# Kernel tuning notes

Hardware: AMD Instinct MI355X
Metric: run time of the kernel (lower is better)

## Reference

```python
import jax, jax.numpy as jnp
import numpy as np

L = 32        # label_num = len(label2idx)
SOS = 0       # label2idx['[SOS]']
END = 1       # label2idx['[END]']
NEG = -10000.0
B, T = 512, 1024


def setup_inputs() -> dict:
    key = jax.random.key(0)
    k1, k2, k3 = jax.random.split(key, 3)
    emission = jax.random.normal(k1, (B, T, L), dtype=jnp.float32)
    label_ids = jax.random.randint(k2, (B, T), 0, L)
    transitions = jax.random.normal(k3, (L, L), dtype=jnp.float32)
    # CrfLayer.__init__: forbid transitions into [SOS] and out of [END]
    transitions = transitions.at[SOS, :].set(NEG).at[:, END].set(NEG)
    return {"emission": emission, "label_ids": label_ids, "transitions": transitions}


def reference(emission, label_ids, transitions):
    b, t, l = emission.shape
    # ---- _forward_alg: log-partition via sequential logsumexp recurrence ----
    alpha0 = jnp.full((b, l), NEG, dtype=emission.dtype).at[:, SOS].set(0.0)
    feats_t = jnp.transpose(emission, (1, 0, 2))  # [T, B, L]

    def step(alpha, feat):
        # aa[b, j, i] = alpha[b, i] + feat[b, j] + transitions[j, i]
        aa = alpha[:, None, :] + feat[:, :, None] + transitions[None, :, :]
        return jax.nn.logsumexp(aa, axis=2), None

    alpha, _ = jax.lax.scan(step, alpha0, feats_t)
    forward_score = jax.nn.logsumexp(alpha + transitions[END][None, :], axis=1)  # [B]

    # ---- _score_sentence: score of the gold path ----
    tags = jnp.concatenate(
        [jnp.full((b, 1), SOS, dtype=label_ids.dtype), label_ids], axis=1)  # [B, T+1]
    trans_score = transitions[tags[:, 1:], tags[:, :-1]].sum(axis=1)          # [B]
    emit_score = jnp.take_along_axis(
        emission, tags[:, 1:, None].astype(jnp.int32), axis=2)[..., 0].sum(axis=1)  # [B]
    gold_score = trans_score + emit_score + transitions[END, tags[:, -1]]

    # loss = sum(forward_score - gold_score)
    return jnp.sum(forward_score - gold_score)
```

## Files before the change

### kernel.cpp

```cpp
#include <hip/hip_runtime.h>


typedef float  f32x16 __attribute__((ext_vector_type(16)));
typedef short  s16x8  __attribute__((ext_vector_type(8)));
typedef float  f32x2  __attribute__((ext_vector_type(2)));
typedef float  f32x4  __attribute__((ext_vector_type(4)));

#define TT 1024
#define LL 32
#define BB 512
#define NW 4
#define CH 8
#define CL 128
#define MS 33

union Frag { s16x8 v; unsigned u[4]; };

__device__ __forceinline__ unsigned pack_bf16(float lo, float hi) {
    return __builtin_amdgcn_perm(__float_as_uint(hi), __float_as_uint(lo), 0x07060302u);
}

__global__ __launch_bounds__(NW * 64, 2) void crf_fused_kernel(
    const float* __restrict__ emission,
    const int*   __restrict__ label_ids,
    const float* __restrict__ transitions,
    float*       __restrict__ out)
{
    __shared__ __align__(16) float shM[CH][32 * MS];
    __shared__ __align__(16) float shF[CH][32];
    __shared__ float shQ[2][64];
    __shared__ float tgArr[NW];
    __shared__ int   capArr[CH];

    const int tid  = threadIdx.x;
    const int w    = tid >> 6;
    const int lane = tid & 63;
    const int j    = lane & 31;
    const int h    = lane >> 5;
    const int b    = blockIdx.x;
    const int t0   = w * (2 * CL);

    {
        const int* labB = label_ids + b * TT + t0;
        float g = 0.0f;
#pragma unroll
        for (int u = 0; u < 4; ++u) {
            int tt = t0 + 64 * u + lane;
            int l1 = labB[64 * u + lane];
            int l0 = (tt == 0) ? 0 : label_ids[b * TT + tt - 1];
            g += transitions[(l1 << 5) + l0];
            g += emission[((size_t)b * TT + tt) * LL + l1];
            if (tt == TT - 1) g += transitions[32 + l1];
        }
#pragma unroll
        for (int m = 32; m >= 1; m >>= 1) g += __shfl_xor(g, m, 64);
        if (lane == 0) tgArr[w] = g;
    }

    const float* trow = transitions + j * 32;
    Frag Ea0, Ea1;
#pragma unroll
    for (int p = 0; p < 4; ++p) {
        int c0 = ((2 * p) & 3)     + 8 * ((2 * p) >> 2)     + 4 * h;
        int c1 = ((2 * p + 1) & 3) + 8 * ((2 * p + 1) >> 2) + 4 * h;
        Ea0.u[p] = pack_bf16(__expf(trow[c0]),      __expf(trow[c1]));
        Ea1.u[p] = pack_bf16(__expf(trow[16 + c0]), __expf(trow[16 + c1]));
    }

    Frag B0a, B1a, B0b, B1b;
#pragma unroll
    for (int i = 0; i < 8; ++i) {
        int row = (i & 3) + 8 * (i >> 2) + 4 * h;
        short lo = (short)((row == j)      ? 0x3F80 : 0);
        short hi = (short)((row + 16 == j) ? 0x3F80 : 0);
        B0a.v[i] = lo;  B1a.v[i] = hi;
        B0b.v[i] = lo;  B1b.v[i] = hi;
    }

    f32x16 zc, accA, accB;
#pragma unroll
    for (int i = 0; i < 16; ++i) zc[i] = 0.0f;

    const float* emA  = emission + ((size_t)b * TT + t0) * LL + j;
    const float* emBp = emA + (size_t)CL * LL;

    float ringA[8], ringB[8];
#pragma unroll
    for (int s = 0; s < 8; ++s) { ringA[s] = emA[s * LL]; ringB[s] = emBp[s * LL]; }

    shF[2 * w][j]     = __expf(ringA[0]);
    shF[2 * w + 1][j] = __expf(ringB[0]);

    float scA = 1.0f, scB = 1.0f;
    int   CapA = 0, elA = 0, CapB = 0, elB = 0;

    auto step = [&](Frag& B0, Frag& B1, f32x16& acc, float (&ring)[8],
                    float& sc, int& Cap, int& elast, const float* em,
                    float* shFc, int cidx, int k, int s, bool refill, bool last) {
        const f32x4* fp = (const f32x4*)shFc;
        f32x4 fA = fp[h], fB = fp[2 + h], fC = fp[4 + h], fD = fp[6 + h];

        acc = __builtin_amdgcn_mfma_f32_32x32x16_bf16(Ea0.v, B0.v, zc, 0, 0, 0);
        acc = __builtin_amdgcn_mfma_f32_32x32x16_bf16(Ea1.v, B1.v, acc, 0, 0, 0);

        if ((s & 3) == 3) {
            int pb = __builtin_amdgcn_readlane(__float_as_int(acc[2]), 0);
            int e  = ((pb >> 23) & 0xff) - 127;
            sc = __int_as_float((127 - e) << 23);
            Cap += e;
            elast = e;
        }

        {
            float fn = __expf(ring[(k + 1) & 7]);
            if (((s + 1) & 3) == 0) fn *= sc;
            shFc[j] = fn;
        }

        if (refill) ring[k] = em[(s + 8) * LL];

        f32x2 t0v[4], t1v[4];
        {
            f32x2 fv, av;
            fv[0] = fA[0]; fv[1] = fA[1]; av[0] = acc[0];  av[1] = acc[1];  t0v[0] = fv * av;
            fv[0] = fA[2]; fv[1] = fA[3]; av[0] = acc[2];  av[1] = acc[3];  t0v[1] = fv * av;
            fv[0] = fB[0]; fv[1] = fB[1]; av[0] = acc[4];  av[1] = acc[5];  t0v[2] = fv * av;
            fv[0] = fB[2]; fv[1] = fB[3]; av[0] = acc[6];  av[1] = acc[7];  t0v[3] = fv * av;
            fv[0] = fC[0]; fv[1] = fC[1]; av[0] = acc[8];  av[1] = acc[9];  t1v[0] = fv * av;
            fv[0] = fC[2]; fv[1] = fC[3]; av[0] = acc[10]; av[1] = acc[11]; t1v[1] = fv * av;
            fv[0] = fD[0]; fv[1] = fD[1]; av[0] = acc[12]; av[1] = acc[13]; t1v[2] = fv * av;
            fv[0] = fD[2]; fv[1] = fD[3]; av[0] = acc[14]; av[1] = acc[15]; t1v[3] = fv * av;
        }
#pragma unroll
        for (int q = 0; q < 4; ++q) {
            B0.u[q] = pack_bf16(t0v[q][0], t0v[q][1]);
            B1.u[q] = pack_bf16(t1v[q][0], t1v[q][1]);
        }

        if (last) {
#pragma unroll
            for (int r = 0; r < 16; ++r) {
                int row = (r & 3) + 8 * (r >> 2) + 4 * h;
                float val = (r < 8) ? t0v[r >> 1][r & 1] : t1v[(r >> 1) - 4][r & 1];
                shM[cidx][row * MS + j] = val;
            }
        }
    };

    for (int s0 = 0; s0 < CL - 8; s0 += 8) {
#pragma unroll
        for (int k = 0; k < 8; ++k) {
            step(B0a, B1a, accA, ringA, scA, CapA, elA, emA,
                 &shF[2 * w][0],     2 * w,     k, s0 + k, true, false);
            step(B0b, B1b, accB, ringB, scB, CapB, elB, emBp,
                 &shF[2 * w + 1][0], 2 * w + 1, k, s0 + k, true, false);
        }
    }
#pragma unroll
    for (int k = 0; k < 8; ++k) {
        step(B0a, B1a, accA, ringA, scA, CapA, elA, emA,
             &shF[2 * w][0],     2 * w,     k, CL - 8 + k, false, k == 7);
        step(B0b, B1b, accB, ringB, scB, CapB, elB, emBp,
             &shF[2 * w + 1][0], 2 * w + 1, k, CL - 8 + k, false, k == 7);
    }

    CapA -= elA;
    CapB -= elB;
    if (lane == 0) { capArr[2 * w] = CapA; capArr[2 * w + 1] = CapB; }

    __syncthreads();

    if (w == 0) {
        const float Eend = __expf(transitions[32 + j]);
        float q = (j == 0) ? 1.0f : 0.0f;
        int   Cq = 0;

#pragma unroll
        for (int c = 0; c < CH; ++c) {
            shQ[c & 1][lane] = q;
            asm volatile("s_waitcnt lgkmcnt(0)" ::: "memory");
            __builtin_amdgcn_wave_barrier();
            const float* Mrow = &shM[c][j * MS];
            const float* qv   = &shQ[c & 1][h * 32];
            float a0 = 0.f, a1 = 0.f, a2 = 0.f, a3 = 0.f;
#pragma unroll
            for (int i = 0; i < 32; i += 4) {
                a0 = fmaf(Mrow[i],     qv[i],     a0);
                a1 = fmaf(Mrow[i + 1], qv[i + 1], a1);
                a2 = fmaf(Mrow[i + 2], qv[i + 2], a2);
                a3 = fmaf(Mrow[i + 3], qv[i + 3], a3);
            }
            float qn = (a0 + a1) + (a2 + a3);
            int pb = __builtin_amdgcn_readlane(__float_as_int(qn), 2);
            int e  = ((pb >> 23) & 0xff) - 127;
            qn *= __int_as_float((127 - e) << 23);
            Cq += e + capArr[c];
            q = qn;
        }

        float gold = 0.0f;
#pragma unroll
        for (int c = 0; c < NW; ++c) gold += tgArr[c];

        float v = q * Eend;
#pragma unroll
        for (int m = 16; m >= 1; m >>= 1) v += __shfl_xor(v, m, 32);
        float fwd = __logf(v) + (float)Cq * 0.69314718055994531f;

        if (lane == 0) atomicAdd(out, fwd - gold);
    }
}

extern "C" void kernel_launch(void* const* d_in, const int* in_sizes, int n_in,
                              void* d_out, int out_size, void* d_ws, size_t ws_size,
                              hipStream_t stream)
{
    const float* emission    = (const float*)d_in[0];
    const int*   label_ids   = (const int*)d_in[1];
    const float* transitions = (const float*)d_in[2];
    float* out = (float*)d_out;

    (void)hipMemsetAsync(out, 0, sizeof(float), stream);
    crf_fused_kernel<<<BB, NW * 64, 0, stream>>>(emission, label_ids, transitions, out);
}
```

Before: 138.6 us.

## Split sequence into 16 chunks across 8 waves with two-phase LDS combine

Doubles the waves per block from 4 to 8 and halves the chunk length to 64 steps, so each block runs 16 independent chunk recurrences in parallel and the serial MFMA chain per wave becomes shorter. To fit the larger block, the per-chunk transfer matrices are kept in registers and written to shared memory in two batches of 8. Wave 0 combines each batch, with extra block barriers between the phases. The trade-offs are more serial combine work, more barriers, and higher occupancy pressure from the launch bound of 4.

```diff
diff --git a/kernel.cpp b/kernel.cpp
--- a/kernel.cpp
+++ b/kernel.cpp
@@ -9,9 +9,10 @@
 #define TT 1024
 #define LL 32
 #define BB 512
-#define NW 4
-#define CH 8
-#define CL 128
+#define NW 8
+#define CH 16
+#define CL 64
+#define NS 8
 #define MS 33
 
 union Frag { s16x8 v; unsigned u[4]; };
@@ -20,13 +21,13 @@
     return __builtin_amdgcn_perm(__float_as_uint(hi), __float_as_uint(lo), 0x07060302u);
 }
 
-__global__ __launch_bounds__(NW * 64, 2) void crf_fused_kernel(
+__global__ __launch_bounds__(NW * 64, 4) void crf_fused_kernel(
     const float* __restrict__ emission,
     const int*   __restrict__ label_ids,
     const float* __restrict__ transitions,
     float*       __restrict__ out)
 {
-    __shared__ __align__(16) float shM[CH][32 * MS];
+    __shared__ __align__(16) float shM[NS][32 * MS];
     __shared__ __align__(16) float shF[CH][32];
     __shared__ float shQ[2][64];
     __shared__ float tgArr[NW];
@@ -44,7 +45,7 @@
         const int* labB = label_ids + b * TT + t0;
         float g = 0.0f;
 #pragma unroll
-        for (int u = 0; u < 4; ++u) {
+        for (int u = 0; u < 2; ++u) {
             int tt = t0 + 64 * u + lane;
             int l1 = labB[64 * u + lane];
             int l0 = (tt == 0) ? 0 : label_ids[b * TT + tt - 1];
@@ -93,10 +94,12 @@
 
     float scA = 1.0f, scB = 1.0f;
     int   CapA = 0, elA = 0, CapB = 0, elB = 0;
+    f32x2 smA0[4], smA1[4], smB0[4], smB1[4];
 
     auto step = [&](Frag& B0, Frag& B1, f32x16& acc, float (&ring)[8],
                     float& sc, int& Cap, int& elast, const float* em,
-                    float* shFc, int cidx, int k, int s, bool refill, bool last) {
+                    float* shFc, f32x2 (&sm0)[4], f32x2 (&sm1)[4],
+                    int k, int s, bool refill, bool last) {
         const f32x4* fp = (const f32x4*)shFc;
         f32x4 fA = fp[h], fB = fp[2 + h], fC = fp[4 + h], fD = fp[6 + h];
 
@@ -139,11 +142,7 @@
 
         if (last) {
 #pragma unroll
-            for (int r = 0; r < 16; ++r) {
-                int row = (r & 3) + 8 * (r >> 2) + 4 * h;
-                float val = (r < 8) ? t0v[r >> 1][r & 1] : t1v[(r >> 1) - 4][r & 1];
-                shM[cidx][row * MS + j] = val;
-            }
+            for (int q = 0; q < 4; ++q) { sm0[q] = t0v[q]; sm1[q] = t1v[q]; }
         }
     };
 
@@ -151,32 +150,39 @@
 #pragma unroll
         for (int k = 0; k < 8; ++k) {
             step(B0a, B1a, accA, ringA, scA, CapA, elA, emA,
-                 &shF[2 * w][0],     2 * w,     k, s0 + k, true, false);
+                 &shF[2 * w][0],     smA0, smA1, k, s0 + k, true, false);
             step(B0b, B1b, accB, ringB, scB, CapB, elB, emBp,
-                 &shF[2 * w + 1][0], 2 * w + 1, k, s0 + k, true, false);
+                 &shF[2 * w + 1][0], smB0, smB1, k, s0 + k, true, false);
         }
     }
 #pragma unroll
     for (int k = 0; k < 8; ++k) {
         step(B0a, B1a, accA, ringA, scA, CapA, elA, emA,
-             &shF[2 * w][0],     2 * w,     k, CL - 8 + k, false, k == 7);
+             &shF[2 * w][0],     smA0, smA1, k, CL - 8 + k, false, k == 7);
         step(B0b, B1b, accB, ringB, scB, CapB, elB, emBp,
-             &shF[2 * w + 1][0], 2 * w + 1, k, CL - 8 + k, false, k == 7);
+             &shF[2 * w + 1][0], smB0, smB1, k, CL - 8 + k, false, k == 7);
     }
 
     CapA -= elA;
     CapB -= elB;
     if (lane == 0) { capArr[2 * w] = CapA; capArr[2 * w + 1] = CapB; }
 
-    __syncthreads();
-
-    if (w == 0) {
-        const float Eend = __expf(transitions[32 + j]);
-        float q = (j == 0) ? 1.0f : 0.0f;
-        int   Cq = 0;
-
-#pragma unroll
-        for (int c = 0; c < CH; ++c) {
+    auto deposit = [&](int slot, f32x2 (&sm0)[4], f32x2 (&sm1)[4]) {
+#pragma unroll
+        for (int r = 0; r < 16; ++r) {
+            int row = (r & 3) + 8 * (r >> 2) + 4 * h;
+            float val = (r < 8) ? sm0[r >> 1][r & 1] : sm1[(r >> 1) - 4][r & 1];
+            shM[slot][row * MS + j] = val;
+        }
+    };
+
+    const float Eend = __expf(transitions[32 + j]);
+    float q  = (j == 0) ? 1.0f : 0.0f;
+    int   Cq = 0;
+
+    auto combine8 = [&](int base) {
+#pragma unroll
+        for (int c = 0; c < NS; ++c) {
             shQ[c & 1][lane] = q;
             asm volatile("s_waitcnt lgkmcnt(0)" ::: "memory");
             __builtin_amdgcn_wave_barrier();
@@ -194,9 +200,25 @@
             int pb = __builtin_amdgcn_readlane(__float_as_int(qn), 2);
             int e  = ((pb >> 23) & 0xff) - 127;
             qn *= __int_as_float((127 - e) << 23);
-            Cq += e + capArr[c];
+            Cq += e + capArr[base + c];
             q = qn;
         }
+    };
+
+    if (w < 4) { deposit(2 * w, smA0, smA1); deposit(2 * w + 1, smB0, smB1); }
+
+    __syncthreads();
+
+    if (w == 0) combine8(0);
+
+    __syncthreads();
+
+    if (w >= 4) { deposit(2 * (w - 4), smA0, smA1); deposit(2 * (w - 4) + 1, smB0, smB1); }
+
+    __syncthreads();
+
+    if (w == 0) {
+        combine8(NS);
 
         float gold = 0.0f;
 #pragma unroll
```

Result: no change. 138.5 us (-0.0%).
